# Optimization experiments

Measured on AMD Instinct MI355X. Metric: run time of the kernel, lower is better.

Reference implementation:

```python
import jax, jax.numpy as jnp
import numpy as np

N = 100000
E = 1600000
IN_CH = 256
HID = 48
OUT_CH = 4
BN_EPS = 1e-5


def setup_inputs() -> dict:
    key = jax.random.key(0)
    ks = jax.random.split(key, 16)
    x = jax.random.normal(ks[0], (N, IN_CH), dtype=jnp.float32)
    edge_index = jax.random.randint(ks[1], (2, E), 0, N, dtype=jnp.int64)
    s = lambda k, shape, fan: jax.random.normal(k, shape, dtype=jnp.float32) / np.sqrt(fan)
    return {
        "x": x,
        "edge_index": edge_index,
        # conv1 (SAGEConv: lin_l on aggregated neighbors w/ bias, lin_r on root, no bias)
        "w1l": s(ks[2], (HID, IN_CH), IN_CH),
        "b1": jnp.zeros((HID,), jnp.float32),
        "w1r": s(ks[3], (HID, IN_CH), IN_CH),
        # bn1 (inference mode: running stats)
        "g1": jnp.ones((HID,), jnp.float32),
        "be1": jnp.zeros((HID,), jnp.float32),
        "rm1": 0.1 * jax.random.normal(ks[4], (HID,), dtype=jnp.float32),
        "rv1": jnp.ones((HID,), jnp.float32) + 0.1 * jax.random.uniform(ks[5], (HID,)),
        # conv2
        "w2l": s(ks[6], (HID, HID), HID),
        "b2": jnp.zeros((HID,), jnp.float32),
        "w2r": s(ks[7], (HID, HID), HID),
        # bn2
        "g2": jnp.ones((HID,), jnp.float32),
        "be2": jnp.zeros((HID,), jnp.float32),
        "rm2": 0.1 * jax.random.normal(ks[8], (HID,), dtype=jnp.float32),
        "rv2": jnp.ones((HID,), jnp.float32) + 0.1 * jax.random.uniform(ks[9], (HID,)),
        # output linear
        "wo": s(ks[10], (OUT_CH, HID), HID),
        "bo": jnp.zeros((OUT_CH,), jnp.float32),
    }


def _sage_conv(h, src, dst, wl, bl, wr, n_nodes):
    # mean-aggregate neighbor features: gather x[src], scatter-sum onto dst, divide by degree
    msgs = h[src]                                             # [E, F] irregular gather
    agg = jax.ops.segment_sum(msgs, dst, num_segments=n_nodes)  # [N, F]
    deg = jax.ops.segment_sum(jnp.ones((src.shape[0],), h.dtype), dst, num_segments=n_nodes)
    mean = agg / jnp.maximum(deg, 1.0)[:, None]
    return mean @ wl.T + bl + h @ wr.T


def _bn_eval(h, g, b, rm, rv):
    return (h - rm) * (g * jax.lax.rsqrt(rv + BN_EPS)) + b


def reference(x, edge_index, w1l, b1, w1r, g1, be1, rm1, rv1,
              w2l, b2, w2r, g2, be2, rm2, rv2, wo, bo):
    src, dst = edge_index[0], edge_index[1]
    n = x.shape[0]
    h = jax.nn.relu(_bn_eval(_sage_conv(x, src, dst, w1l, b1, w1r, n), g1, be1, rm1, rv1))
    h = jax.nn.relu(_bn_eval(_sage_conv(h, src, dst, w2l, b2, w2r, n), g2, be2, rm2, rv2))
    return h @ wo.T + bo
```

## Files before the change

kernel.cpp:

```cpp
#include <hip/hip_runtime.h>
#include <hip/hip_bf16.h>

#define N_NODES 100000
#define N_EDGES 1600000
#define IN_CH   256
#define BN_EPS  1e-5f
#define SCAN_NB 98
#define NPART   8
#define PART_SZ 12500
#define NGRP    800

typedef __attribute__((ext_vector_type(8))) short bf16x8;
typedef __attribute__((ext_vector_type(4))) float f32x4;
typedef __attribute__((ext_vector_type(4))) int   i32x4;

__device__ inline unsigned f2bf(float x) {
    unsigned u = __float_as_uint(x);
    return (u + 0x7fffu + ((u >> 16) & 1u)) >> 16;
}
__device__ inline unsigned pk2(float x, float y) {
    return f2bf(x) | (f2bf(y) << 16);
}
__device__ inline bf16x8 pack8(float4 a, float4 b) {
    i32x4 r;
    r.x = (int)pk2(a.x, a.y); r.y = (int)pk2(a.z, a.w);
    r.z = (int)pk2(b.x, b.y); r.w = (int)pk2(b.z, b.w);
    return __builtin_bit_cast(bf16x8, r);
}
__device__ inline float lo16(unsigned u) { return __uint_as_float(u << 16); }
__device__ inline float hi16(unsigned u) { return __uint_as_float(u & 0xffff0000u); }

__global__ __launch_bounds__(256) void hist_part(const int* __restrict__ ei, int* __restrict__ cnt) {
    int p = blockIdx.x & (NPART - 1);
    int g = blockIdx.x >> 3;
    int lo = p * PART_SZ, hi = lo + PART_SZ;
    int e0 = (g * 256 + (int)threadIdx.x) * 8;
    if (e0 >= N_EDGES) return;
    const i32x4* dp = (const i32x4*)(ei + N_EDGES + e0);
    i32x4 d0 = __builtin_nontemporal_load(dp);
    i32x4 d1 = __builtin_nontemporal_load(dp + 1);
    int d[8] = {d0.x, d0.y, d0.z, d0.w, d1.x, d1.y, d1.z, d1.w};
#pragma unroll
    for (int j = 0; j < 8; j++)
        if (d[j] >= lo && d[j] < hi) atomicAdd(&cnt[d[j]], 1);
}

__global__ __launch_bounds__(256) void scatter_part(const int* __restrict__ ei, int* __restrict__ cur,
                                                    int* __restrict__ csr) {
    int p = blockIdx.x & (NPART - 1);
    int g = blockIdx.x >> 3;
    int lo = p * PART_SZ, hi = lo + PART_SZ;
    int e0 = (g * 256 + (int)threadIdx.x) * 8;
    if (e0 >= N_EDGES) return;
    const i32x4* dp = (const i32x4*)(ei + N_EDGES + e0);
    const i32x4* sp = (const i32x4*)(ei + e0);
    i32x4 d0 = __builtin_nontemporal_load(dp);
    i32x4 d1 = __builtin_nontemporal_load(dp + 1);
    i32x4 s0 = __builtin_nontemporal_load(sp);
    i32x4 s1 = __builtin_nontemporal_load(sp + 1);
    int d[8] = {d0.x, d0.y, d0.z, d0.w, d1.x, d1.y, d1.z, d1.w};
    int s[8] = {s0.x, s0.y, s0.z, s0.w, s1.x, s1.y, s1.z, s1.w};
#pragma unroll
    for (int j = 0; j < 8; j++) {
        if (d[j] >= lo && d[j] < hi && (unsigned)s[j] < N_NODES) {
            int pos = atomicAdd(&cur[d[j]], 1);
            csr[pos] = s[j];
        }
    }
}

__global__ __launch_bounds__(256) void scan_k1(const int* __restrict__ cnt, int* __restrict__ bsum) {
    __shared__ int lds[256];
    int b = blockIdx.x, t = threadIdx.x;
    int i0 = b * 1024 + t * 4;
    int s = 0;
#pragma unroll
    for (int j = 0; j < 4; j++) { int i = i0 + j; if (i < N_NODES) s += cnt[i]; }
    lds[t] = s; __syncthreads();
    for (int o = 128; o; o >>= 1) { if (t < o) lds[t] += lds[t + o]; __syncthreads(); }
    if (t == 0) bsum[b] = lds[0];
}

__global__ void scan_k2(const int* __restrict__ bsum, int* __restrict__ bex, int nb) {
    __shared__ int lds[128];
    int t = threadIdx.x;
    int v = (t < nb) ? bsum[t] : 0;
    lds[t] = v; __syncthreads();
    for (int o = 1; o < 128; o <<= 1) {
        int u = (t >= o) ? lds[t - o] : 0;
        __syncthreads();
        lds[t] += u;
        __syncthreads();
    }
    if (t < nb) bex[t] = lds[t] - v;
}

__global__ __launch_bounds__(256) void scan_k3(const int* __restrict__ cnt, const int* __restrict__ bex,
                                               int* __restrict__ off, int* __restrict__ cur) {
    __shared__ int lds[256];
    int b = blockIdx.x, t = threadIdx.x;
    int i0 = b * 1024 + t * 4;
    int c[4]; int s = 0;
#pragma unroll
    for (int j = 0; j < 4; j++) { int i = i0 + j; c[j] = (i < N_NODES) ? cnt[i] : 0; s += c[j]; }
    lds[t] = s; __syncthreads();
    for (int o = 1; o < 256; o <<= 1) {
        int u = (t >= o) ? lds[t - o] : 0;
        __syncthreads();
        lds[t] += u;
        __syncthreads();
    }
    int ex = lds[t] - s + bex[b];
#pragma unroll
    for (int j = 0; j < 4; j++) {
        int i = i0 + j;
        if (i < N_NODES) { off[i] = ex; cur[i] = ex; ex += c[j]; }
    }
}

__global__ __launch_bounds__(256) void gemm1_mfma(const float* __restrict__ in,
        const float* __restrict__ W0, const float* __restrict__ W1,
        __hip_bfloat16* __restrict__ P, float* __restrict__ R) {
    __shared__ bf16x8 wlds[8 * 6 * 64];
    int tid = threadIdx.x;
    for (int s = tid; s < 8 * 6 * 64; s += 256) {
        int lane = s & 63, tile = (s >> 6) % 6, kstep = s / 384;
        int c = tile * 16 + (lane & 15);
        int k0 = kstep * 32 + (lane >> 4) * 8;
        const float* Wp = (c < 48) ? &W0[(size_t)c * IN_CH] : &W1[(size_t)(c - 48) * IN_CH];
        float4 a = *(const float4*)&Wp[k0];
        float4 b = *(const float4*)&Wp[k0 + 4];
        wlds[s] = pack8(a, b);
    }
    __syncthreads();

    int w = tid >> 6, lane = tid & 63;
    int lr = lane & 15, kq = lane >> 4;
    int rbase = blockIdx.x * 128 + w * 32;
    f32x4 acc[2][6] = {};

    for (int kstep = 0; kstep < 8; kstep++) {
        int kb = kstep * 32 + kq * 8;
        bf16x8 afr[2] = {};
#pragma unroll
        for (int mt = 0; mt < 2; mt++) {
            int row = rbase + mt * 16 + lr;
            if (row < N_NODES) {
                const float* ip = &in[(size_t)row * IN_CH + kb];
                afr[mt] = pack8(*(const float4*)ip, *(const float4*)(ip + 4));
            }
        }
        bf16x8 bfr[6];
#pragma unroll
        for (int t = 0; t < 6; t++) bfr[t] = wlds[(kstep * 6 + t) * 64 + lane];
#pragma unroll
        for (int t = 0; t < 6; t++)
#pragma unroll
            for (int mt = 0; mt < 2; mt++)
                acc[mt][t] = __builtin_amdgcn_mfma_f32_16x16x32_bf16(afr[mt], bfr[t], acc[mt][t], 0, 0, 0);
    }
#pragma unroll
    for (int mt = 0; mt < 2; mt++)
#pragma unroll
        for (int t = 0; t < 6; t++)
#pragma unroll
            for (int j = 0; j < 4; j++) {
                int row = rbase + mt * 16 + kq * 4 + j;
                if (row < N_NODES) {
                    float v = acc[mt][t][j];
                    int col = t * 16 + lr;
                    if (t < 3) P[(size_t)row * 48 + col] = __float2bfloat16(v);
                    else       R[(size_t)row * 48 + (col - 48)] = v;
                }
            }
}

__global__ __launch_bounds__(256) void gemm2_mfma(const __hip_bfloat16* __restrict__ inb,
        const float* __restrict__ W0, const float* __restrict__ W1,
        __hip_bfloat16* __restrict__ P, float* __restrict__ R) {
    __shared__ bf16x8 wlds[2 * 6 * 64];
    int tid = threadIdx.x;
    for (int s = tid; s < 2 * 6 * 64; s += 256) {
        int lane = s & 63, tile = (s >> 6) % 6, kstep = s / 384;
        int c = tile * 16 + (lane & 15);
        int k0 = kstep * 32 + (lane >> 4) * 8;
        const float* Wp = (c < 48) ? &W0[(size_t)c * 48] : &W1[(size_t)(c - 48) * 48];
        float v[8];
#pragma unroll
        for (int j = 0; j < 8; j++) { int k = k0 + j; v[j] = (k < 48) ? Wp[k] : 0.f; }
        wlds[s] = pack8(make_float4(v[0], v[1], v[2], v[3]), make_float4(v[4], v[5], v[6], v[7]));
    }
    __syncthreads();

    int w = tid >> 6, lane = tid & 63;
    int lr = lane & 15, kq = lane >> 4;
    int rbase = blockIdx.x * 128 + w * 32;
    f32x4 acc[2][6] = {};

    for (int kstep = 0; kstep < 2; kstep++) {
        int kb = kstep * 32 + kq * 8;
        bf16x8 afr[2] = {};
#pragma unroll
        for (int mt = 0; mt < 2; mt++) {
            int row = rbase + mt * 16 + lr;
            if (row < N_NODES)
                afr[mt] = *(const bf16x8*)&inb[(size_t)row * 64 + kb];
        }
        bf16x8 bfr[6];
#pragma unroll
        for (int t = 0; t < 6; t++) bfr[t] = wlds[(kstep * 6 + t) * 64 + lane];
#pragma unroll
        for (int t = 0; t < 6; t++)
#pragma unroll
            for (int mt = 0; mt < 2; mt++)
                acc[mt][t] = __builtin_amdgcn_mfma_f32_16x16x32_bf16(afr[mt], bfr[t], acc[mt][t], 0, 0, 0);
    }
#pragma unroll
    for (int mt = 0; mt < 2; mt++)
#pragma unroll
        for (int t = 0; t < 6; t++)
#pragma unroll
            for (int j = 0; j < 4; j++) {
                int row = rbase + mt * 16 + kq * 4 + j;
                if (row < N_NODES) {
                    float v = acc[mt][t][j];
                    int col = t * 16 + lr;
                    if (t < 3) P[(size_t)row * 48 + col] = __float2bfloat16(v);
                    else       R[(size_t)row * 48 + (col - 48)] = v;
                }
            }
}

__global__ __launch_bounds__(256) void agg_csr_b16(const int* __restrict__ off, const int* __restrict__ cnt,
                                                   const int* __restrict__ csr,
                                                   const unsigned* __restrict__ P32,
                                                   float* __restrict__ agg) {
    int t = blockIdx.x * blockDim.x + threadIdx.x;
    int node = t >> 3, l = t & 7;
    if (node >= N_NODES) return;
    int s = off[node], len = cnt[node];
    float a0 = 0.f, a1 = 0.f, a2 = 0.f, a3 = 0.f, a4 = 0.f, a5 = 0.f;
    int i = 0;
    for (; i + 4 <= len; i += 4) {
        int sx[4];
#pragma unroll
        for (int q = 0; q < 4; q++) sx[q] = csr[s + i + q];
        unsigned uu[4][3];
#pragma unroll
        for (int q = 0; q < 4; q++) {
            const unsigned* p = P32 + (size_t)sx[q] * 24 + l;
            uu[q][0] = p[0]; uu[q][1] = p[8]; uu[q][2] = p[16];
        }
#pragma unroll
        for (int q = 0; q < 4; q++) {
            a0 += lo16(uu[q][0]); a1 += hi16(uu[q][0]);
            a2 += lo16(uu[q][1]); a3 += hi16(uu[q][1]);
            a4 += lo16(uu[q][2]); a5 += hi16(uu[q][2]);
        }
    }
    for (; i < len; i++) {
        const unsigned* p = P32 + (size_t)csr[s + i] * 24 + l;
        unsigned u0 = p[0], u1 = p[8], u2 = p[16];
        a0 += lo16(u0); a1 += hi16(u0);
        a2 += lo16(u1); a3 += hi16(u1);
        a4 += lo16(u2); a5 += hi16(u2);
    }
    size_t base = (size_t)node * 48;
    *(float2*)&agg[base +  0 + 2 * l] = make_float2(a0, a1);
    *(float2*)&agg[base + 16 + 2 * l] = make_float2(a2, a3);
    *(float2*)&agg[base + 32 + 2 * l] = make_float2(a4, a5);
}

__global__ void post1_kernel(const float* __restrict__ agg, const int* __restrict__ cnt,
                             const float* __restrict__ R,
                             const float* __restrict__ b,  const float* __restrict__ g,
                             const float* __restrict__ be, const float* __restrict__ rm,
                             const float* __restrict__ rv, __hip_bfloat16* __restrict__ h) {
    int t = blockIdx.x * blockDim.x + threadIdx.x;
    if (t >= N_NODES * 48) return;
    int n = t / 48, j = t % 48;
    float mean = agg[t] / fmaxf((float)cnt[n], 1.0f);
    float v = mean + b[j] + R[t];
    v = (v - rm[j]) * (g[j] * rsqrtf(rv[j] + BN_EPS)) + be[j];
    h[(size_t)n * 64 + j] = __float2bfloat16(fmaxf(v, 0.0f));
}

__global__ void out_kernel(const float* __restrict__ agg, const int* __restrict__ cnt,
                           const float* __restrict__ R,
                           const float* __restrict__ b2, const float* __restrict__ g2,
                           const float* __restrict__ be2, const float* __restrict__ rm2,
                           const float* __restrict__ rv2,
                           const float* __restrict__ wo, const float* __restrict__ bo,
                           float* __restrict__ out) {
    int t = blockIdx.x * blockDim.x + threadIdx.x;
    int node = t >> 4, l = t & 15;
    if (node >= N_NODES) return;
    float dg = fmaxf((float)cnt[node], 1.0f);
    float p0 = 0.f, p1 = 0.f, p2 = 0.f, p3 = 0.f;
#pragma unroll
    for (int q = 0; q < 3; q++) {
        int j = l + q * 16;
        float v = agg[(size_t)node * 48 + j] / dg + b2[j] + R[(size_t)node * 48 + j];
        v = (v - rm2[j]) * (g2[j] * rsqrtf(rv2[j] + BN_EPS)) + be2[j];
        v = fmaxf(v, 0.f);
        p0 = fmaf(v, wo[0 * 48 + j], p0);
        p1 = fmaf(v, wo[1 * 48 + j], p1);
        p2 = fmaf(v, wo[2 * 48 + j], p2);
        p3 = fmaf(v, wo[3 * 48 + j], p3);
    }
#pragma unroll
    for (int offm = 8; offm; offm >>= 1) {
        p0 += __shfl_down(p0, offm, 16);
        p1 += __shfl_down(p1, offm, 16);
        p2 += __shfl_down(p2, offm, 16);
        p3 += __shfl_down(p3, offm, 16);
    }
    if (l == 0) {
        float4 o = make_float4(p0 + bo[0], p1 + bo[1], p2 + bo[2], p3 + bo[3]);
        *(float4*)&out[(size_t)node * 4] = o;
    }
}

extern "C" void kernel_launch(void* const* d_in, const int* in_sizes, int n_in,
                              void* d_out, int out_size, void* d_ws, size_t ws_size,
                              hipStream_t stream) {
    const float* x   = (const float*)d_in[0];
    const int*   ei  = (const int*)d_in[1];
    const float* w1l = (const float*)d_in[2];
    const float* b1  = (const float*)d_in[3];
    const float* w1r = (const float*)d_in[4];
    const float* g1  = (const float*)d_in[5];
    const float* be1 = (const float*)d_in[6];
    const float* rm1 = (const float*)d_in[7];
    const float* rv1 = (const float*)d_in[8];
    const float* w2l = (const float*)d_in[9];
    const float* b2  = (const float*)d_in[10];
    const float* w2r = (const float*)d_in[11];
    const float* g2  = (const float*)d_in[12];
    const float* be2 = (const float*)d_in[13];
    const float* rm2 = (const float*)d_in[14];
    const float* rv2 = (const float*)d_in[15];
    const float* wo  = (const float*)d_in[16];
    const float* bo  = (const float*)d_in[17];
    float* out = (float*)d_out;

    char* w = (char*)d_ws;
    float*           Rbuf = (float*)w;                       w += (size_t)N_NODES * 48 * 4;
    float*           AGG  = (float*)w;                       w += (size_t)N_NODES * 48 * 4;
    __hip_bfloat16*  P    = (__hip_bfloat16*)w;              w += (size_t)N_NODES * 48 * 2;
    __hip_bfloat16*  H1   = (__hip_bfloat16*)w;              w += (size_t)N_NODES * 64 * 2;
    int*             CNT  = (int*)w;                         w += (size_t)N_NODES * 4;
    int*             OFF  = (int*)w;                         w += (size_t)N_NODES * 4;
    int*             CUR  = (int*)w;                         w += (size_t)N_NODES * 4;
    int*             BSUM = (int*)w;                         w += 128 * 4;
    int*             BEX  = (int*)w;                         w += 128 * 4;
    int*             CSR  = (int*)w;

    (void)hipMemsetAsync(CNT, 0, N_NODES * sizeof(int), stream);
    (void)hipMemsetAsync(H1, 0, (size_t)N_NODES * 64 * 2, stream);

    hist_part<<<NPART * NGRP, 256, 0, stream>>>(ei, CNT);
    scan_k1<<<SCAN_NB, 256, 0, stream>>>(CNT, BSUM);
    scan_k2<<<1, 128, 0, stream>>>(BSUM, BEX, SCAN_NB);
    scan_k3<<<SCAN_NB, 256, 0, stream>>>(CNT, BEX, OFF, CUR);
    scatter_part<<<NPART * NGRP, 256, 0, stream>>>(ei, CUR, CSR);

    gemm1_mfma<<<(N_NODES + 127) / 128, 256, 0, stream>>>(x, w1l, w1r, P, Rbuf);
    agg_csr_b16<<<(N_NODES * 8 + 255) / 256, 256, 0, stream>>>(OFF, CNT, CSR, (const unsigned*)P, AGG);
    post1_kernel<<<(N_NODES * 48 + 255) / 256, 256, 0, stream>>>(AGG, CNT, Rbuf,
                                                                 b1, g1, be1, rm1, rv1, H1);

    gemm2_mfma<<<(N_NODES + 127) / 128, 256, 0, stream>>>(H1, w2l, w2r, P, Rbuf);
    agg_csr_b16<<<(N_NODES * 8 + 255) / 256, 256, 0, stream>>>(OFF, CNT, CSR, (const unsigned*)P, AGG);
    out_kernel<<<(N_NODES * 16 + 255) / 256, 256, 0, stream>>>(AGG, CNT, Rbuf,
                                                               b2, g2, be2, rm2, rv2,
                                                               wo, bo, out);
}
```

Measured before the change: 476.6 us.

## Prepack GEMM weights once, prefetch A tiles, drop nontemporal edge loads

Adds a small wpack kernel that converts both layers' weights into MFMA fragment layout in bf16 once per call. The GEMM kernels then read those fragments straight from global memory (cached) instead of rebuilding an LDS copy in every block behind a barrier. gemm1 also software-prefetches the next k-step's input rows into registers and clamps row indices so the loads need no branch. The edge-list loads in hist/scatter switch from nontemporal to normal loads, likely so the repeated reads across partitions can hit in cache. This adds two tiny kernel launches and more register pressure in gemm1.

```diff
diff --git a/kernel.cpp b/kernel.cpp
--- a/kernel.cpp
+++ b/kernel.cpp
@@ -37,8 +37,8 @@
     int e0 = (g * 256 + (int)threadIdx.x) * 8;
     if (e0 >= N_EDGES) return;
     const i32x4* dp = (const i32x4*)(ei + N_EDGES + e0);
-    i32x4 d0 = __builtin_nontemporal_load(dp);
-    i32x4 d1 = __builtin_nontemporal_load(dp + 1);
+    i32x4 d0 = dp[0];
+    i32x4 d1 = dp[1];
     int d[8] = {d0.x, d0.y, d0.z, d0.w, d1.x, d1.y, d1.z, d1.w};
 #pragma unroll
     for (int j = 0; j < 8; j++)
@@ -54,10 +54,10 @@
     if (e0 >= N_EDGES) return;
     const i32x4* dp = (const i32x4*)(ei + N_EDGES + e0);
     const i32x4* sp = (const i32x4*)(ei + e0);
-    i32x4 d0 = __builtin_nontemporal_load(dp);
-    i32x4 d1 = __builtin_nontemporal_load(dp + 1);
-    i32x4 s0 = __builtin_nontemporal_load(sp);
-    i32x4 s1 = __builtin_nontemporal_load(sp + 1);
+    i32x4 d0 = dp[0];
+    i32x4 d1 = dp[1];
+    i32x4 s0 = sp[0];
+    i32x4 s1 = sp[1];
     int d[8] = {d0.x, d0.y, d0.z, d0.w, d1.x, d1.y, d1.z, d1.w};
     int s[8] = {s0.x, s0.y, s0.z, s0.w, s1.x, s1.y, s1.z, s1.w};
 #pragma unroll
@@ -118,46 +118,57 @@
     }
 }
 
+__global__ void wpack(const float* __restrict__ W0, const float* __restrict__ W1,
+                      int K, int nfrag, i32x4* __restrict__ WF) {
+    int s = blockIdx.x * blockDim.x + threadIdx.x;
+    if (s >= nfrag) return;
+    int lane = s & 63, tile = (s >> 6) % 6, kstep = s / 384;
+    int c = tile * 16 + (lane & 15);
+    int k0 = kstep * 32 + (lane >> 4) * 8;
+    const float* Wp = (c < 48) ? &W0[(size_t)c * K] : &W1[(size_t)(c - 48) * K];
+    float v[8];
+#pragma unroll
+    for (int j = 0; j < 8; j++) { int k = k0 + j; v[j] = (k < K) ? Wp[k] : 0.f; }
+    WF[s] = __builtin_bit_cast(i32x4, pack8(make_float4(v[0], v[1], v[2], v[3]),
+                                            make_float4(v[4], v[5], v[6], v[7])));
+}
+
 __global__ __launch_bounds__(256) void gemm1_mfma(const float* __restrict__ in,
-        const float* __restrict__ W0, const float* __restrict__ W1,
+        const i32x4* __restrict__ WF,
         __hip_bfloat16* __restrict__ P, float* __restrict__ R) {
-    __shared__ bf16x8 wlds[8 * 6 * 64];
     int tid = threadIdx.x;
-    for (int s = tid; s < 8 * 6 * 64; s += 256) {
-        int lane = s & 63, tile = (s >> 6) % 6, kstep = s / 384;
-        int c = tile * 16 + (lane & 15);
-        int k0 = kstep * 32 + (lane >> 4) * 8;
-        const float* Wp = (c < 48) ? &W0[(size_t)c * IN_CH] : &W1[(size_t)(c - 48) * IN_CH];
-        float4 a = *(const float4*)&Wp[k0];
-        float4 b = *(const float4*)&Wp[k0 + 4];
-        wlds[s] = pack8(a, b);
-    }
-    __syncthreads();
-
     int w = tid >> 6, lane = tid & 63;
     int lr = lane & 15, kq = lane >> 4;
     int rbase = blockIdx.x * 128 + w * 32;
+    int r0 = rbase + lr, r1 = rbase + 16 + lr;
+    const float* ap0 = in + (size_t)(r0 < N_NODES ? r0 : N_NODES - 1) * IN_CH;
+    const float* ap1 = in + (size_t)(r1 < N_NODES ? r1 : N_NODES - 1) * IN_CH;
+
     f32x4 acc[2][6] = {};
+    float4 c0a = *(const float4*)(ap0 + kq * 8);
+    float4 c0b = *(const float4*)(ap0 + kq * 8 + 4);
+    float4 c1a = *(const float4*)(ap1 + kq * 8);
+    float4 c1b = *(const float4*)(ap1 + kq * 8 + 4);
 
     for (int kstep = 0; kstep < 8; kstep++) {
-        int kb = kstep * 32 + kq * 8;
-        bf16x8 afr[2] = {};
-#pragma unroll
-        for (int mt = 0; mt < 2; mt++) {
-            int row = rbase + mt * 16 + lr;
-            if (row < N_NODES) {
-                const float* ip = &in[(size_t)row * IN_CH + kb];
-                afr[mt] = pack8(*(const float4*)ip, *(const float4*)(ip + 4));
-            }
-        }
-        bf16x8 bfr[6];
-#pragma unroll
-        for (int t = 0; t < 6; t++) bfr[t] = wlds[(kstep * 6 + t) * 64 + lane];
-#pragma unroll
-        for (int t = 0; t < 6; t++)
-#pragma unroll
-            for (int mt = 0; mt < 2; mt++)
-                acc[mt][t] = __builtin_amdgcn_mfma_f32_16x16x32_bf16(afr[mt], bfr[t], acc[mt][t], 0, 0, 0);
+        i32x4 bf[6];
+#pragma unroll
+        for (int t = 0; t < 6; t++) bf[t] = WF[(kstep * 6 + t) * 64 + lane];
+        float4 n0a, n0b, n1a, n1b;
+        if (kstep < 7) {
+            int kb = (kstep + 1) * 32 + kq * 8;
+            n0a = *(const float4*)(ap0 + kb); n0b = *(const float4*)(ap0 + kb + 4);
+            n1a = *(const float4*)(ap1 + kb); n1b = *(const float4*)(ap1 + kb + 4);
+        }
+        bf16x8 af0 = pack8(c0a, c0b);
+        bf16x8 af1 = pack8(c1a, c1b);
+#pragma unroll
+        for (int t = 0; t < 6; t++) {
+            bf16x8 bfr = __builtin_bit_cast(bf16x8, bf[t]);
+            acc[0][t] = __builtin_amdgcn_mfma_f32_16x16x32_bf16(af0, bfr, acc[0][t], 0, 0, 0);
+            acc[1][t] = __builtin_amdgcn_mfma_f32_16x16x32_bf16(af1, bfr, acc[1][t], 0, 0, 0);
+        }
+        if (kstep < 7) { c0a = n0a; c0b = n0b; c1a = n1a; c1b = n1b; }
     }
 #pragma unroll
     for (int mt = 0; mt < 2; mt++)
@@ -176,44 +187,31 @@
 }
 
 __global__ __launch_bounds__(256) void gemm2_mfma(const __hip_bfloat16* __restrict__ inb,
-        const float* __restrict__ W0, const float* __restrict__ W1,
+        const i32x4* __restrict__ WF,
         __hip_bfloat16* __restrict__ P, float* __restrict__ R) {
-    __shared__ bf16x8 wlds[2 * 6 * 64];
     int tid = threadIdx.x;
-    for (int s = tid; s < 2 * 6 * 64; s += 256) {
-        int lane = s & 63, tile = (s >> 6) % 6, kstep = s / 384;
-        int c = tile * 16 + (lane & 15);
-        int k0 = kstep * 32 + (lane >> 4) * 8;
-        const float* Wp = (c < 48) ? &W0[(size_t)c * 48] : &W1[(size_t)(c - 48) * 48];
-        float v[8];
-#pragma unroll
-        for (int j = 0; j < 8; j++) { int k = k0 + j; v[j] = (k < 48) ? Wp[k] : 0.f; }
-        wlds[s] = pack8(make_float4(v[0], v[1], v[2], v[3]), make_float4(v[4], v[5], v[6], v[7]));
-    }
-    __syncthreads();
-
     int w = tid >> 6, lane = tid & 63;
     int lr = lane & 15, kq = lane >> 4;
     int rbase = blockIdx.x * 128 + w * 32;
+    int r0 = rbase + lr, r1 = rbase + 16 + lr;
+    const __hip_bfloat16* ap0 = inb + (size_t)(r0 < N_NODES ? r0 : N_NODES - 1) * 64;
+    const __hip_bfloat16* ap1 = inb + (size_t)(r1 < N_NODES ? r1 : N_NODES - 1) * 64;
+
     f32x4 acc[2][6] = {};
-
+#pragma unroll
     for (int kstep = 0; kstep < 2; kstep++) {
         int kb = kstep * 32 + kq * 8;
-        bf16x8 afr[2] = {};
-#pragma unroll
-        for (int mt = 0; mt < 2; mt++) {
-            int row = rbase + mt * 16 + lr;
-            if (row < N_NODES)
-                afr[mt] = *(const bf16x8*)&inb[(size_t)row * 64 + kb];
-        }
-        bf16x8 bfr[6];
-#pragma unroll
-        for (int t = 0; t < 6; t++) bfr[t] = wlds[(kstep * 6 + t) * 64 + lane];
-#pragma unroll
-        for (int t = 0; t < 6; t++)
-#pragma unroll
-            for (int mt = 0; mt < 2; mt++)
-                acc[mt][t] = __builtin_amdgcn_mfma_f32_16x16x32_bf16(afr[mt], bfr[t], acc[mt][t], 0, 0, 0);
+        bf16x8 af0 = *(const bf16x8*)(ap0 + kb);
+        bf16x8 af1 = *(const bf16x8*)(ap1 + kb);
+        i32x4 bf[6];
+#pragma unroll
+        for (int t = 0; t < 6; t++) bf[t] = WF[(kstep * 6 + t) * 64 + lane];
+#pragma unroll
+        for (int t = 0; t < 6; t++) {
+            bf16x8 bfr = __builtin_bit_cast(bf16x8, bf[t]);
+            acc[0][t] = __builtin_amdgcn_mfma_f32_16x16x32_bf16(af0, bfr, acc[0][t], 0, 0, 0);
+            acc[1][t] = __builtin_amdgcn_mfma_f32_16x16x32_bf16(af1, bfr, acc[1][t], 0, 0, 0);
+        }
     }
 #pragma unroll
     for (int mt = 0; mt < 2; mt++)
@@ -354,10 +352,15 @@
     int*             CUR  = (int*)w;                         w += (size_t)N_NODES * 4;
     int*             BSUM = (int*)w;                         w += 128 * 4;
     int*             BEX  = (int*)w;                         w += 128 * 4;
+    i32x4*           WF1  = (i32x4*)w;                       w += 3072 * 16;
+    i32x4*           WF2  = (i32x4*)w;                       w += 768 * 16;
     int*             CSR  = (int*)w;
 
     (void)hipMemsetAsync(CNT, 0, N_NODES * sizeof(int), stream);
     (void)hipMemsetAsync(H1, 0, (size_t)N_NODES * 64 * 2, stream);
+
+    wpack<<<12, 256, 0, stream>>>(w1l, w1r, IN_CH, 3072, WF1);
+    wpack<<<3, 256, 0, stream>>>(w2l, w2r, 48, 768, WF2);
 
     hist_part<<<NPART * NGRP, 256, 0, stream>>>(ei, CNT);
     scan_k1<<<SCAN_NB, 256, 0, stream>>>(CNT, BSUM);
@@ -365,12 +368,12 @@
     scan_k3<<<SCAN_NB, 256, 0, stream>>>(CNT, BEX, OFF, CUR);
     scatter_part<<<NPART * NGRP, 256, 0, stream>>>(ei, CUR, CSR);
 
-    gemm1_mfma<<<(N_NODES + 127) / 128, 256, 0, stream>>>(x, w1l, w1r, P, Rbuf);
+    gemm1_mfma<<<(N_NODES + 127) / 128, 256, 0, stream>>>(x, WF1, P, Rbuf);
     agg_csr_b16<<<(N_NODES * 8 + 255) / 256, 256, 0, stream>>>(OFF, CNT, CSR, (const unsigned*)P, AGG);
     post1_kernel<<<(N_NODES * 48 + 255) / 256, 256, 0, stream>>>(AGG, CNT, Rbuf,
                                                                  b1, g1, be1, rm1, rv1, H1);
 
-    gemm2_mfma<<<(N_NODES + 127) / 128, 256, 0, stream>>>(H1, w2l, w2r, P, Rbuf);
+    gemm2_mfma<<<(N_NODES + 127) / 128, 256, 0, stream>>>(H1, WF2, P, Rbuf);
     agg_csr_b16<<<(N_NODES * 8 + 255) / 256, 256, 0, stream>>>(OFF, CNT, CSR, (const unsigned*)P, AGG);
     out_kernel<<<(N_NODES * 16 + 255) / 256, 256, 0, stream>>>(AGG, CNT, Rbuf,
                                                                b2, g2, be2, rm2, rv2,
```

Result: faster. 457.3 us (-4.0%).
